# Optimization experiments

Hardware: AMD Instinct MI355X
Metric: run time of the kernel (lower is better)

Reference implementation:

```python
import jax, jax.numpy as jnp
import numpy as np

jax.config.update("jax_enable_x64", True)

N_NODES = 100000
E0 = 3_200_000
EN = 3_200_000


def setup_inputs() -> dict:
    key = jax.random.key(0)
    k1, k2 = jax.random.split(key)
    A0 = jax.random.randint(k1, (2, E0), 0, N_NODES, dtype=jnp.int64)
    An = jax.random.randint(k2, (2, EN), 0, N_NODES, dtype=jnp.int64)
    p = jnp.float32(0.1)  # learned scalar parameter
    return {"A0_edge_index": A0, "An_edge_index": An, "ver": 1, "p": p}


def reference(A0_edge_index, An_edge_index, ver, p):
    if ver == 1:
        keep_prob = jax.nn.sigmoid(p)
        e0 = A0_edge_index.shape[1]
        # Bernoulli keep-mask over A0 edges (fixed key for determinism)
        mask = jax.random.bernoulli(jax.random.key(42), keep_prob, (e0,))
        SHIFT = jnp.int64(1) << 32  # pack (src,dst) into one int64 code
        SENT = jnp.iinfo(jnp.int64).max
        a0_codes = A0_edge_index[0] * SHIFT + A0_edge_index[1]
        a0_codes = jnp.where(mask, a0_codes, SENT)  # dropped edges -> sentinel
        an_codes = An_edge_index[0] * SHIFT + An_edge_index[1]
        codes = jnp.concatenate([a0_codes, an_codes])
        # sort-based dedup; fixed output size, padded with sentinel
        uniq = jnp.unique(codes, size=codes.shape[0], fill_value=SENT)
        valid = uniq != SENT
        src = jnp.where(valid, uniq // SHIFT, -1)
        dst = jnp.where(valid, uniq % SHIFT, -1)
        return jnp.stack([src, dst])  # [2, E0+EN], padded cols are -1
    else:
        w = jax.nn.sigmoid(p)
        return w * A0_edge_index + (1.0 - w) * An_edge_index
```

## Files before the change

### kernel.cpp

```cpp
#include <hip/hip_runtime.h>
#include <stdint.h>

#define BUK 782
#define CAP 6912
#define CH  8192
#define SENTK 0xFFFFFFFFu

__device__ __forceinline__ uint32_t rotl32(uint32_t x, int r) { return (x << r) | (x >> (32 - r)); }

__device__ __forceinline__ uint32_t threefry_bits(uint32_t i) {
  const uint32_t k0 = 0u, k1 = 42u;
  const uint32_t k2 = k0 ^ k1 ^ 0x1BD11BDAu;
  uint32_t x0 = k0;
  uint32_t x1 = i + k1;
#define TF_R(r) { x0 += x1; x1 = rotl32(x1, r); x1 ^= x0; }
  TF_R(13) TF_R(15) TF_R(26) TF_R(6)   x0 += k1; x1 += k2 + 1u;
  TF_R(17) TF_R(29) TF_R(16) TF_R(24)  x0 += k2; x1 += k0 + 2u;
  TF_R(13) TF_R(15) TF_R(26) TF_R(6)   x0 += k0; x1 += k1 + 3u;
  TF_R(17) TF_R(29) TF_R(16) TF_R(24)  x0 += k1; x1 += k2 + 4u;
  TF_R(13) TF_R(15) TF_R(26) TF_R(6)   x0 += k2; x1 += k0 + 5u;
#undef TF_R
  return x0 ^ x1;
}

__device__ __forceinline__ bool keep_edge(uint32_t i, float kp) {
  uint32_t bits = threefry_bits(i);
  float u = __uint_as_float((bits >> 9) | 0x3f800000u) - 1.0f;
  return u < kp;
}

__device__ __forceinline__ float keep_prob(const float* pp) {
  double pd = (double)pp[0];
  return (float)(1.0 / (1.0 + exp(-pd)));
}

template <int J>
__device__ __forceinline__ uint32_t xshf(uint32_t v, int lane) {
  if constexpr (J == 1) {
    return (uint32_t)__builtin_amdgcn_mov_dpp((int)v, 0xB1, 0xF, 0xF, true);
  } else if constexpr (J == 2) {
    return (uint32_t)__builtin_amdgcn_mov_dpp((int)v, 0x4E, 0xF, 0xF, true);
  } else if constexpr (J == 4 || J == 8) {
    uint32_t up = (uint32_t)__builtin_amdgcn_mov_dpp((int)v, 0x100 | J, 0xF, 0xF, true);
    uint32_t dn = (uint32_t)__builtin_amdgcn_mov_dpp((int)v, 0x110 | J, 0xF, 0xF, true);
    return (lane & J) ? dn : up;
  } else {
    return (uint32_t)__shfl_xor((int)v, J, 64);
  }
}

__device__ __forceinline__ void cex(uint32_t& v, uint32_t o, bool takeMin) {
  uint32_t mn = v < o ? v : o, mx = v < o ? o : v;
  v = takeMin ? mn : mx;
}
template <int J>
__device__ __forceinline__ void ce1(uint32_t& v, bool takeMin, int lane) {
  cex(v, xshf<J>(v, lane), takeMin);
}

__device__ __forceinline__ uint32_t bitonic64(uint32_t v, int lane) {
#define BS1(J, K) ce1<J>(v, ((lane & (J)) == 0) == ((lane & (K)) == 0), lane)
  BS1(1, 2);
  BS1(2, 4); BS1(1, 4);
  BS1(4, 8); BS1(2, 8); BS1(1, 8);
  BS1(8, 16); BS1(4, 16); BS1(2, 16); BS1(1, 16);
  BS1(16, 32); BS1(8, 32); BS1(4, 32); BS1(2, 32); BS1(1, 32);
  ce1<32>(v, (lane & 32) == 0, lane); ce1<16>(v, (lane & 16) == 0, lane);
  ce1<8>(v, (lane & 8) == 0, lane);   ce1<4>(v, (lane & 4) == 0, lane);
  ce1<2>(v, (lane & 2) == 0, lane);   ce1<1>(v, (lane & 1) == 0, lane);
#undef BS1
  return v;
}

__device__ __forceinline__ void bitonic128(uint32_t& v0, uint32_t& v1, int lane) {
#define BS2(J, K) { bool tm = ((lane & (J)) == 0) == ((lane & (K)) == 0); ce1<J>(v0, tm, lane); ce1<J>(v1, tm, lane); }
  BS2(1, 2);
  BS2(2, 4); BS2(1, 4);
  BS2(4, 8); BS2(2, 8); BS2(1, 8);
  BS2(8, 16); BS2(4, 16); BS2(2, 16); BS2(1, 16);
  BS2(16, 32); BS2(8, 32); BS2(4, 32); BS2(2, 32); BS2(1, 32);
#undef BS2
  ce1<32>(v0, (lane & 32) == 0, lane); ce1<32>(v1, (lane & 32) != 0, lane);
  ce1<16>(v0, (lane & 16) == 0, lane); ce1<16>(v1, (lane & 16) != 0, lane);
  ce1<8>(v0, (lane & 8) == 0, lane);   ce1<8>(v1, (lane & 8) != 0, lane);
  ce1<4>(v0, (lane & 4) == 0, lane);   ce1<4>(v1, (lane & 4) != 0, lane);
  ce1<2>(v0, (lane & 2) == 0, lane);   ce1<2>(v1, (lane & 2) != 0, lane);
  ce1<1>(v0, (lane & 1) == 0, lane);   ce1<1>(v1, (lane & 1) != 0, lane);
  { uint32_t lo = v0 < v1 ? v0 : v1, hi = v0 < v1 ? v1 : v0; v0 = lo; v1 = hi; }
  ce1<32>(v0, (lane & 32) == 0, lane); ce1<32>(v1, (lane & 32) == 0, lane);
  ce1<16>(v0, (lane & 16) == 0, lane); ce1<16>(v1, (lane & 16) == 0, lane);
  ce1<8>(v0, (lane & 8) == 0, lane);   ce1<8>(v1, (lane & 8) == 0, lane);
  ce1<4>(v0, (lane & 4) == 0, lane);   ce1<4>(v1, (lane & 4) == 0, lane);
  ce1<2>(v0, (lane & 2) == 0, lane);   ce1<2>(v1, (lane & 2) == 0, lane);
  ce1<1>(v0, (lane & 1) == 0, lane);   ce1<1>(v1, (lane & 1) == 0, lane);
}

__global__ __launch_bounds__(512) void passA_k(const int* __restrict__ a0,
                                               const int* __restrict__ an,
                                               int e0, int en, const float* __restrict__ pp,
                                               uint32_t* __restrict__ cur_g,
                                               uint32_t* __restrict__ bkt) {
  __shared__ uint32_t stageK[CH];
  __shared__ uint16_t stageB[CH];
  __shared__ uint32_t cntA[784];
  __shared__ uint32_t loA[784];
  __shared__ uint32_t gb[784];
  __shared__ uint32_t sums[512];

  float kp = keep_prob(pp);
  int tid = threadIdx.x;
  int total = e0 + en;
  int base = blockIdx.x * CH;

  uint32_t key[16];
  uint32_t bkid[16];

  for (int t = tid; t < 784; t += 512) cntA[t] = 0;
  __syncthreads();

#pragma unroll
  for (int k = 0; k < 4; k++) {
    int g = base + 4 * (k * 512 + tid);
    int s4[4], d4[4];
    bool have = false;
    if (g + 3 < e0) {
      int4 sv = *reinterpret_cast<const int4*>(&a0[g]);
      int4 dv = *reinterpret_cast<const int4*>(&a0[e0 + g]);
      s4[0] = sv.x; s4[1] = sv.y; s4[2] = sv.z; s4[3] = sv.w;
      d4[0] = dv.x; d4[1] = dv.y; d4[2] = dv.z; d4[3] = dv.w;
      have = true;
    } else if (g >= e0 && g + 3 < total) {
      int j = g - e0;
      int4 sv = *reinterpret_cast<const int4*>(&an[j]);
      int4 dv = *reinterpret_cast<const int4*>(&an[en + j]);
      s4[0] = sv.x; s4[1] = sv.y; s4[2] = sv.z; s4[3] = sv.w;
      d4[0] = dv.x; d4[1] = dv.y; d4[2] = dv.z; d4[3] = dv.w;
      have = true;
    } else if (g < total) {
      for (int e = 0; e < 4; e++) {
        int idx = g + e;
        if (idx < total) {
          if (idx < e0) { s4[e] = a0[idx]; d4[e] = a0[e0 + idx]; }
          else          { int j = idx - e0; s4[e] = an[j]; d4[e] = an[en + j]; }
        } else { s4[e] = -1; d4[e] = 0; }
      }
      have = true;
    }
#pragma unroll
    for (int e = 0; e < 4; e++) {
      int idx = g + e;
      uint32_t ky = SENTK, b_ = SENTK;
      if (have && idx < total && s4[e] >= 0) {
        bool keep = (idx < e0) ? keep_edge((uint32_t)idx, kp) : true;
        if (keep) {
          uint32_t us = (uint32_t)s4[e];
          b_ = us >> 7;
          if (b_ < BUK) ky = ((us & 127u) << 17) | (uint32_t)d4[e];
          else b_ = SENTK;
        }
      }
      key[k * 4 + e] = ky;
      bkid[k * 4 + e] = b_;
      if (b_ != SENTK) atomicAdd(&cntA[b_], 1u);
    }
  }
  __syncthreads();

  {
    uint32_t s2 = 0;
    if (tid < 392) s2 = cntA[2 * tid] + cntA[2 * tid + 1];
    sums[tid] = s2;
    __syncthreads();
    for (int off = 1; off < 512; off <<= 1) {
      uint32_t a = (tid >= off) ? sums[tid - off] : 0u;
      __syncthreads();
      sums[tid] += a;
      __syncthreads();
    }
    if (tid < 392) {
      uint32_t b0 = sums[tid] - s2;
      loA[2 * tid] = b0;
      loA[2 * tid + 1] = b0 + cntA[2 * tid];
    }
  }
  __syncthreads();
  for (int t = tid; t < 784; t += 512) gb[t] = loA[t];
  __syncthreads();

#pragma unroll
  for (int k = 0; k < 16; k++) {
    uint32_t b_ = bkid[k];
    if (b_ != SENTK) {
      uint32_t p = atomicAdd(&gb[b_], 1u);
      stageK[p] = key[k];
      stageB[p] = (uint16_t)b_;
    }
  }
  __syncthreads();

  for (int t = tid; t < BUK; t += 512) {
    uint32_t c = gb[t] - loA[t];
    gb[t] = c ? atomicAdd(&cur_g[t], c) : 0u;
  }
  __syncthreads();

  uint32_t kept = sums[511];
  for (uint32_t i = tid; i < kept; i += 512) {
    uint32_t b_ = stageB[i];
    uint32_t addr = gb[b_] + (i - loA[b_]);
    if (addr < CAP) bkt[(size_t)b_ * CAP + addr] = stageK[i];
  }
}

__global__ __launch_bounds__(512) void passB_k(uint32_t* __restrict__ bkt,
                                               const uint32_t* __restrict__ cur_g,
                                               uint32_t* __restrict__ ucnt) {
  __shared__ uint32_t lin[CAP];
  __shared__ uint32_t c128[128], lo128[128], cur128[128];
  __shared__ uint32_t u128[128], uo128[128];

  int b = blockIdx.x, tid = threadIdx.x;
  int wid = tid >> 6, lane = tid & 63;
  uint32_t len = cur_g[b];
  if (len > CAP) len = CAP;
  uint32_t* seg = bkt + (size_t)b * CAP;

  if (tid < 128) c128[tid] = 0;
  __syncthreads();

  uint32_t rv[16];
#pragma unroll
  for (int k = 0; k < 4; k++) {
    uint32_t i4 = 4u * (uint32_t)(k * 512 + tid);
    if (i4 + 3 < len) {
      uint4 v = *reinterpret_cast<const uint4*>(&seg[i4]);
      rv[4 * k] = v.x; rv[4 * k + 1] = v.y; rv[4 * k + 2] = v.z; rv[4 * k + 3] = v.w;
    } else {
#pragma unroll
      for (int e = 0; e < 4; e++) rv[4 * k + e] = (i4 + e < len) ? seg[i4 + e] : SENTK;
    }
  }

#pragma unroll
  for (int k = 0; k < 16; k++)
    if (rv[k] != SENTK) atomicAdd(&c128[rv[k] >> 17], 1u);
  __syncthreads();

  if (tid < 128) lo128[tid] = c128[tid];
  __syncthreads();
  for (int off = 1; off < 128; off <<= 1) {
    uint32_t a = 0;
    if (tid < 128 && tid >= off) a = lo128[tid - off];
    __syncthreads();
    if (tid < 128) lo128[tid] += a;
    __syncthreads();
  }
  if (tid < 128) {
    uint32_t ex = lo128[tid] - c128[tid];
    lo128[tid] = ex;
    cur128[tid] = ex;
  }
  __syncthreads();

#pragma unroll
  for (int k = 0; k < 16; k++)
    if (rv[k] != SENTK) lin[atomicAdd(&cur128[rv[k] >> 17], 1u)] = rv[k];
  __syncthreads();

  for (int s = wid; s < 128; s += 8) {
    uint32_t L = c128[s], sb = lo128[s];
    if (L > 1u && L <= 64u) {
      uint32_t v = (lane < (int)L) ? lin[sb + lane] : SENTK;
      v = bitonic64(v, lane);
      if (lane < (int)L) lin[sb + lane] = v;
    } else if (L > 64u && L <= 128u) {
      uint32_t v0 = (lane < (int)L) ? lin[sb + lane] : SENTK;
      uint32_t v1 = (64 + lane < (int)L) ? lin[sb + 64 + lane] : SENTK;
      bitonic128(v0, v1, lane);
      if (lane < (int)L) lin[sb + lane] = v0;
      if (64 + lane < (int)L) lin[sb + 64 + lane] = v1;
    } else if (L > 128u) {
      uint32_t* gsc = seg + sb;
      for (uint32_t i0 = lane; i0 < L; i0 += 64) {
        uint32_t x = lin[sb + i0];
        uint32_t pos = 0;
        for (uint32_t j = 0; j < L; j++) {
          uint32_t y = lin[sb + j];
          pos += (y < x || (y == x && j < i0)) ? 1u : 0u;
        }
        gsc[pos] = x;
      }
      asm volatile("s_waitcnt vmcnt(0)" ::: "memory");
      for (uint32_t i0 = lane; i0 < L; i0 += 64) lin[sb + i0] = gsc[i0];
    }
    uint32_t ub = 0;
    for (uint32_t t = 0; t < L; t += 64) {
      uint32_t i = t + lane;
      bool valid = i < L;
      uint32_t x = valid ? lin[sb + i] : 0u;
      uint32_t prev = valid ? lin[sb + (i == 0 ? 0 : i - 1)] : 0u;
      bool uniq = valid && (i == 0 || prev != x);
      unsigned long long ball = __ballot(uniq ? 1 : 0);
      uint32_t rank = (uint32_t)__popcll(ball & ((1ull << lane) - 1ull));
      if (uniq) lin[sb + ub + rank] = x;
      ub += (uint32_t)__popcll(ball);
    }
    if (lane == 0) u128[s] = ub;
  }
  __syncthreads();

  if (tid < 128) uo128[tid] = u128[tid];
  __syncthreads();
  for (int off = 1; off < 128; off <<= 1) {
    uint32_t a = 0;
    if (tid < 128 && tid >= off) a = uo128[tid - off];
    __syncthreads();
    if (tid < 128) uo128[tid] += a;
    __syncthreads();
  }
  if (tid < 128) uo128[tid] -= u128[tid];
  __syncthreads();

  for (int s = wid; s < 128; s += 8) {
    uint32_t u = u128[s], sb = lo128[s], ob = uo128[s];
    for (uint32_t k2 = lane; k2 < u; k2 += 64) seg[ob + k2] = lin[sb + k2];
  }
  if (tid == 0) ucnt[b] = uo128[127] + u128[127];
}

__global__ __launch_bounds__(1024) void uscan_k(const uint32_t* __restrict__ ucnt,
                                                uint32_t* __restrict__ uoff) {
  __shared__ uint32_t s[1024];
  int t = threadIdx.x;
  uint32_t v = (t < BUK) ? ucnt[t] : 0u;
  s[t] = v;
  __syncthreads();
  for (int off = 1; off < 1024; off <<= 1) {
    uint32_t a = (t >= off) ? s[t - off] : 0u;
    __syncthreads();
    s[t] += a;
    __syncthreads();
  }
  if (t <= BUK) uoff[t] = s[t] - v;
}

__global__ __launch_bounds__(256) void passC_k(const uint32_t* __restrict__ bkt,
                                               const uint32_t* __restrict__ uoff,
                                               int* __restrict__ out, int oute) {
  int b = blockIdx.x;
  uint32_t lo = uoff[b], u = uoff[b + 1] - lo;
  const uint32_t* seg = bkt + (size_t)b * CAP;
  for (uint32_t k = threadIdx.x; k < u; k += 256) {
    uint32_t key = seg[k];
    out[lo + k] = (int)((uint32_t)(b << 7) | (key >> 17));
    out[oute + lo + k] = (int)(key & 0x1FFFFu);
  }
}

__global__ void tail_k(const uint32_t* __restrict__ uoff, int* __restrict__ out, int oute) {
  uint32_t total = uoff[BUK];
  for (uint32_t i = blockIdx.x * blockDim.x + threadIdx.x + total; i < (uint32_t)oute;
       i += gridDim.x * blockDim.x) {
    out[i] = -1;
    out[oute + i] = -1;
  }
}

extern "C" void kernel_launch(void* const* d_in, const int* in_sizes, int n_in,
                              void* d_out, int out_size, void* d_ws, size_t ws_size,
                              hipStream_t stream) {
  const int* a0 = (const int*)d_in[0];
  const int* an = (const int*)d_in[1];
  const float* pp = (const float*)d_in[3];
  int e0 = in_sizes[0] / 2;
  int en = in_sizes[1] / 2;
  int M = e0 + en;
  int oute = out_size / 2;

  uint8_t* wbase = (uint8_t*)d_ws;
  size_t o = 0;
  auto nxt = [&](size_t bytes) -> void* {
    void* p = wbase + o;
    o = (o + bytes + 255) & ~(size_t)255;
    return p;
  };
  uint32_t* cur_g = (uint32_t*)nxt((size_t)BUK * 4);
  uint32_t* ucnt  = (uint32_t*)nxt((size_t)BUK * 4);
  uint32_t* uoff  = (uint32_t*)nxt((size_t)(BUK + 1) * 4);
  uint32_t* bkt   = (uint32_t*)nxt((size_t)BUK * CAP * 4);

  int ablocks = (M + CH - 1) / CH;

  hipMemsetAsync(cur_g, 0, (size_t)BUK * 4, stream);
  passA_k<<<ablocks, 512, 0, stream>>>(a0, an, e0, en, pp, cur_g, bkt);
  passB_k<<<BUK, 512, 0, stream>>>(bkt, cur_g, ucnt);
  uscan_k<<<1, 1024, 0, stream>>>(ucnt, uoff);
  passC_k<<<BUK, 256, 0, stream>>>(bkt, uoff, (int*)d_out, oute);
  tail_k<<<1024, 256, 0, stream>>>(uoff, (int*)d_out, oute);
}
```

Before: 112.4 us.

## Use wave-level shuffle scans, pad global bucket counters, simplify passA scatter

The barrier-heavy shared-memory block scans in passA, passB and uscan are replaced by single-wave shuffle scans, with each lane handling several elements sequentially. The global per-bucket counters are spread 16 words apart so atomics from different blocks on neighbouring buckets do not share a cache line. passA drops the stageB bucket-id array and now has one thread per bucket copy that bucket's staged keys to global memory in a serial loop. This removes many __syncthreads and some LDS use, but the per-thread serial scatter may coalesce worse than the old strided copy loop.

```diff
diff --git a/kernel.cpp b/kernel.cpp
--- a/kernel.cpp
+++ b/kernel.cpp
@@ -4,6 +4,7 @@
 #define BUK 782
 #define CAP 6912
 #define CH  8192
+#define PAD 16
 #define SENTK 0xFFFFFFFFu
 
 __device__ __forceinline__ uint32_t rotl32(uint32_t x, int r) { return (x << r) | (x >> (32 - r)); }
@@ -32,6 +33,15 @@
 __device__ __forceinline__ float keep_prob(const float* pp) {
   double pd = (double)pp[0];
   return (float)(1.0 / (1.0 + exp(-pd)));
+}
+
+__device__ __forceinline__ uint32_t wave_incl_scan(uint32_t v, int lane) {
+#pragma unroll
+  for (int off = 1; off < 64; off <<= 1) {
+    uint32_t t = (uint32_t)__shfl_up((int)v, off, 64);
+    if (lane >= off) v += t;
+  }
+  return v;
 }
 
 template <int J>
@@ -101,14 +111,13 @@
                                                uint32_t* __restrict__ cur_g,
                                                uint32_t* __restrict__ bkt) {
   __shared__ uint32_t stageK[CH];
-  __shared__ uint16_t stageB[CH];
   __shared__ uint32_t cntA[784];
   __shared__ uint32_t loA[784];
   __shared__ uint32_t gb[784];
-  __shared__ uint32_t sums[512];
 
   float kp = keep_prob(pp);
   int tid = threadIdx.x;
+  int wid = tid >> 6, lane = tid & 63;
   int total = e0 + en;
   int base = blockIdx.x * CH;
 
@@ -166,49 +175,44 @@
   }
   __syncthreads();
 
-  {
-    uint32_t s2 = 0;
-    if (tid < 392) s2 = cntA[2 * tid] + cntA[2 * tid + 1];
-    sums[tid] = s2;
-    __syncthreads();
-    for (int off = 1; off < 512; off <<= 1) {
-      uint32_t a = (tid >= off) ? sums[tid - off] : 0u;
-      __syncthreads();
-      sums[tid] += a;
-      __syncthreads();
-    }
-    if (tid < 392) {
-      uint32_t b0 = sums[tid] - s2;
-      loA[2 * tid] = b0;
-      loA[2 * tid + 1] = b0 + cntA[2 * tid];
-    }
-  }
-  __syncthreads();
-  for (int t = tid; t < 784; t += 512) gb[t] = loA[t];
+  if (wid == 0) {
+    uint32_t c[13];
+    uint32_t s = 0;
+#pragma unroll
+    for (int j = 0; j < 13; j++) {
+      int idx = lane * 13 + j;
+      c[j] = (idx < 784) ? cntA[idx] : 0u;
+      s += c[j];
+    }
+    uint32_t inc = wave_incl_scan(s, lane);
+    uint32_t ex = inc - s;
+#pragma unroll
+    for (int j = 0; j < 13; j++) {
+      int idx = lane * 13 + j;
+      if (idx < 784) { loA[idx] = ex; gb[idx] = ex; }
+      ex += c[j];
+    }
+  }
   __syncthreads();
 
 #pragma unroll
   for (int k = 0; k < 16; k++) {
     uint32_t b_ = bkid[k];
-    if (b_ != SENTK) {
-      uint32_t p = atomicAdd(&gb[b_], 1u);
-      stageK[p] = key[k];
-      stageB[p] = (uint16_t)b_;
-    }
+    if (b_ != SENTK) stageK[atomicAdd(&gb[b_], 1u)] = key[k];
   }
   __syncthreads();
 
   for (int t = tid; t < BUK; t += 512) {
-    uint32_t c = gb[t] - loA[t];
-    gb[t] = c ? atomicAdd(&cur_g[t], c) : 0u;
-  }
-  __syncthreads();
-
-  uint32_t kept = sums[511];
-  for (uint32_t i = tid; i < kept; i += 512) {
-    uint32_t b_ = stageB[i];
-    uint32_t addr = gb[b_] + (i - loA[b_]);
-    if (addr < CAP) bkt[(size_t)b_ * CAP + addr] = stageK[i];
+    uint32_t c = cntA[t];
+    if (c) {
+      uint32_t gbase = atomicAdd(&cur_g[(size_t)t * PAD], c);
+      uint32_t lo = loA[t];
+      uint32_t* dstp = bkt + (size_t)t * CAP;
+      for (uint32_t j = 0; j < c; j++) {
+        uint32_t a = gbase + j;
+        if (a < CAP) dstp[a] = stageK[lo + j];
+      }
+    }
   }
 }
 
@@ -221,7 +225,7 @@
 
   int b = blockIdx.x, tid = threadIdx.x;
   int wid = tid >> 6, lane = tid & 63;
-  uint32_t len = cur_g[b];
+  uint32_t len = cur_g[(size_t)b * PAD];
   if (len > CAP) len = CAP;
   uint32_t* seg = bkt + (size_t)b * CAP;
 
@@ -246,19 +250,13 @@
     if (rv[k] != SENTK) atomicAdd(&c128[rv[k] >> 17], 1u);
   __syncthreads();
 
-  if (tid < 128) lo128[tid] = c128[tid];
-  __syncthreads();
-  for (int off = 1; off < 128; off <<= 1) {
-    uint32_t a = 0;
-    if (tid < 128 && tid >= off) a = lo128[tid - off];
-    __syncthreads();
-    if (tid < 128) lo128[tid] += a;
-    __syncthreads();
-  }
-  if (tid < 128) {
-    uint32_t ex = lo128[tid] - c128[tid];
-    lo128[tid] = ex;
-    cur128[tid] = ex;
+  if (wid == 0) {
+    uint32_t c0 = c128[2 * lane], c1 = c128[2 * lane + 1];
+    uint32_t s = c0 + c1;
+    uint32_t inc = wave_incl_scan(s, lane);
+    uint32_t ex = inc - s;
+    lo128[2 * lane] = ex;       lo128[2 * lane + 1] = ex + c0;
+    cur128[2 * lane] = ex;      cur128[2 * lane + 1] = ex + c0;
   }
   __syncthreads();
 
@@ -309,39 +307,42 @@
   }
   __syncthreads();
 
-  if (tid < 128) uo128[tid] = u128[tid];
-  __syncthreads();
-  for (int off = 1; off < 128; off <<= 1) {
-    uint32_t a = 0;
-    if (tid < 128 && tid >= off) a = uo128[tid - off];
-    __syncthreads();
-    if (tid < 128) uo128[tid] += a;
-    __syncthreads();
-  }
-  if (tid < 128) uo128[tid] -= u128[tid];
+  if (wid == 0) {
+    uint32_t c0 = u128[2 * lane], c1 = u128[2 * lane + 1];
+    uint32_t s = c0 + c1;
+    uint32_t inc = wave_incl_scan(s, lane);
+    uint32_t ex = inc - s;
+    uo128[2 * lane] = ex;       uo128[2 * lane + 1] = ex + c0;
+    if (lane == 63) ucnt[b] = inc;
+  }
   __syncthreads();
 
   for (int s = wid; s < 128; s += 8) {
     uint32_t u = u128[s], sb = lo128[s], ob = uo128[s];
     for (uint32_t k2 = lane; k2 < u; k2 += 64) seg[ob + k2] = lin[sb + k2];
   }
-  if (tid == 0) ucnt[b] = uo128[127] + u128[127];
-}
-
-__global__ __launch_bounds__(1024) void uscan_k(const uint32_t* __restrict__ ucnt,
-                                                uint32_t* __restrict__ uoff) {
-  __shared__ uint32_t s[1024];
-  int t = threadIdx.x;
-  uint32_t v = (t < BUK) ? ucnt[t] : 0u;
-  s[t] = v;
-  __syncthreads();
-  for (int off = 1; off < 1024; off <<= 1) {
-    uint32_t a = (t >= off) ? s[t - off] : 0u;
-    __syncthreads();
-    s[t] += a;
-    __syncthreads();
-  }
-  if (t <= BUK) uoff[t] = s[t] - v;
+}
+
+__global__ __launch_bounds__(64) void uscan_k(const uint32_t* __restrict__ ucnt,
+                                              uint32_t* __restrict__ uoff) {
+  int lane = threadIdx.x;
+  uint32_t c[13];
+  uint32_t s = 0;
+#pragma unroll
+  for (int j = 0; j < 13; j++) {
+    int idx = lane * 13 + j;
+    c[j] = (idx < BUK) ? ucnt[idx] : 0u;
+    s += c[j];
+  }
+  uint32_t inc = wave_incl_scan(s, lane);
+  uint32_t ex = inc - s;
+#pragma unroll
+  for (int j = 0; j < 13; j++) {
+    int idx = lane * 13 + j;
+    if (idx < BUK) uoff[idx] = ex;
+    ex += c[j];
+  }
+  if (lane == 63) uoff[BUK] = inc;
 }
 
 __global__ __launch_bounds__(256) void passC_k(const uint32_t* __restrict__ bkt,
@@ -384,17 +385,17 @@
     o = (o + bytes + 255) & ~(size_t)255;
     return p;
   };
-  uint32_t* cur_g = (uint32_t*)nxt((size_t)BUK * 4);
+  uint32_t* cur_g = (uint32_t*)nxt((size_t)BUK * PAD * 4);
   uint32_t* ucnt  = (uint32_t*)nxt((size_t)BUK * 4);
   uint32_t* uoff  = (uint32_t*)nxt((size_t)(BUK + 1) * 4);
   uint32_t* bkt   = (uint32_t*)nxt((size_t)BUK * CAP * 4);
 
   int ablocks = (M + CH - 1) / CH;
 
-  hipMemsetAsync(cur_g, 0, (size_t)BUK * 4, stream);
+  hipMemsetAsync(cur_g, 0, (size_t)BUK * PAD * 4, stream);
   passA_k<<<ablocks, 512, 0, stream>>>(a0, an, e0, en, pp, cur_g, bkt);
   passB_k<<<BUK, 512, 0, stream>>>(bkt, cur_g, ucnt);
-  uscan_k<<<1, 1024, 0, stream>>>(ucnt, uoff);
+  uscan_k<<<1, 64, 0, stream>>>(ucnt, uoff);
   passC_k<<<BUK, 256, 0, stream>>>(bkt, uoff, (int*)d_out, oute);
   tail_k<<<1024, 256, 0, stream>>>(uoff, (int*)d_out, oute);
 }
```

After: 130.7 us. 1.16x slower.
